# Optimization experiments

Hardware: AMD Instinct MI355X
Metric: run time of the kernel (lower is better)

## Reference

```python
import jax, jax.numpy as jnp
import numpy as np

B, N, S = 8, 4096, 1024          # clouds, points per cloud, fps samples per cloud
C_IN = 64
R_LIST = (0.1, 0.2, 0.4)
K_LIST = (16, 32, 64)
CHANNELS = ([C_IN + 3, 64, 64, 128], [C_IN + 3, 128, 128, 256], [C_IN + 3, 128, 128, 256])


def setup_inputs() -> dict:
    key = jax.random.key(0)
    ks = jax.random.split(key, 2 + 9)
    inp = {}
    inp["x"] = jax.random.normal(ks[0], (B * N, C_IN), jnp.float32)
    inp["pos"] = jax.random.uniform(ks[1], (B * N, 3), jnp.float32)
    inp["batch"] = jnp.repeat(jnp.arange(B, dtype=jnp.int32), N)
    ki = 2
    for s, ch in enumerate(CHANNELS):
        for l in range(len(ch) - 1):
            inp[f"W{s}_{l}"] = jax.random.normal(ks[ki], (ch[l], ch[l + 1]), jnp.float32) / np.float32(np.sqrt(ch[l]))
            inp[f"b{s}_{l}"] = jnp.zeros((ch[l + 1],), jnp.float32)
        ki += 1
    return inp


def _fps_one(pos_b):
    """Farthest point sampling on one cloud [N,3] -> [S] int32 indices (start at 0)."""
    def step(carry, _):
        min_d, last = carry
        d = jnp.sum((pos_b - pos_b[last]) ** 2, axis=-1)          # [N]
        min_d = jnp.minimum(min_d, d)
        return (min_d, jnp.argmax(min_d).astype(jnp.int32)), last
    init = (jnp.full((N,), jnp.inf, pos_b.dtype), jnp.int32(0))
    _, idx = jax.lax.scan(step, init, None, length=S)
    return idx


def _scale(xb, posb, centers, r, K, Ws, bs):
    """Radius ball query (K nearest within r) + PointConv (MLP on [x_j, pos_j-pos_i], max-aggr)."""
    d2 = jnp.sum((centers[:, None, :] - posb[None, :, :]) ** 2, axis=-1)  # [S,N]
    neg = jnp.where(d2 <= r * r, -d2, -jnp.inf)
    vals, nbr = jax.lax.top_k(neg, K)                                      # [S,K]
    valid = vals > -jnp.inf                                                # center itself always valid
    feat = jnp.concatenate([xb[nbr], posb[nbr] - centers[:, None, :]], axis=-1)  # [S,K,C+3]
    h = feat
    for W, b in zip(Ws, bs):
        h = jax.nn.relu(h @ W + b)
    h = jnp.where(valid[..., None], h, -jnp.inf)
    return jnp.max(h, axis=1)                                              # [S,out]


def _forward(x, pos, batch, params):
    xb = x.reshape(B, N, C_IN)
    posb = pos.reshape(B, N, 3)
    idx = jax.vmap(_fps_one)(posb)                                # [B,S]
    centers = jnp.take_along_axis(posb, idx[..., None], axis=1)   # [B,S,3]
    outs = []
    for s in range(3):
        Ws, bs = params[s]
        f = lambda xb_, pb_, c_, Ws=Ws, bs=bs, s=s: _scale(xb_, pb_, c_, R_LIST[s], K_LIST[s], Ws, bs)
        outs.append(jax.vmap(f)(xb, posb, centers))
    new_x = jnp.concatenate(outs, axis=-1).reshape(B * S, -1)     # [B*S, 640]
    new_pos = centers.reshape(B * S, 3)
    new_batch = jnp.repeat(jnp.arange(B, dtype=batch.dtype), S)
    return new_x, new_pos, new_batch


def reference(x, pos, batch, W0_0, b0_0, W0_1, b0_1, W0_2, b0_2,
              W1_0, b1_0, W1_1, b1_1, W1_2, b1_2,
              W2_0, b2_0, W2_1, b2_1, W2_2, b2_2):
    params = (((W0_0, W0_1, W0_2), (b0_0, b0_1, b0_2)),
              ((W1_0, W1_1, W1_2), (b1_0, b1_1, b1_2)),
              ((W2_0, W2_1, W2_2), (b2_0, b2_1, b2_2)))
    return _forward(x, pos, batch, params)
```

## Files before the change

### kernel.cpp

```cpp
#include <hip/hip_runtime.h>

#define NB 8
#define NP 4096
#define NS 1024
#define PROGSTRIDE 32

typedef _Float16 f16x8 __attribute__((ext_vector_type(8)));
typedef _Float16 f16x4 __attribute__((ext_vector_type(4)));
typedef float f32x4 __attribute__((ext_vector_type(4)));

#define DPP_MAX(v, ctrl)                                                     \
    v = fmaxf(v, __int_as_float(__builtin_amdgcn_update_dpp(                 \
                __float_as_int(v), __float_as_int(v), (ctrl), 0xf, 0xf, false)))

struct PrepArgs {
    const float* src[9];
    _Float16* dst[9];
    int kr[9], kp[9], nc[9];
};

template <int K>
__device__ __forceinline__ void select_center(
        const float* __restrict__ pb,
        const float* __restrict__ centers,
        int* __restrict__ nbr, int* __restrict__ nvalid,
        float r2, int scid) {
#pragma clang fp contract(off)
    const int lane = threadIdx.x & 63;
    const unsigned kr2 = __float_as_uint(r2);
    const float cx = centers[scid * 3 + 0];
    const float cy = centers[scid * 3 + 1];
    const float cz = centers[scid * 3 + 2];

    unsigned key[64];
#pragma unroll
    for (int i = 0; i < 64; ++i) {
        const float* pp = pb + (size_t)(lane + i * 64) * 3;
        float dx = pp[0] - cx; float sx = dx * dx;
        float dy = pp[1] - cy; float sy = dy * dy;
        float dz = pp[2] - cz; float sz = dz * dz;
        float d2 = sx + sy; d2 = d2 + sz;
        key[i] = __float_as_uint(d2);
    }

    const unsigned long long below = (1ull << lane) - 1ull;
    int c_cnt = 0;
#pragma unroll
    for (int i = 0; i < 64; ++i)
        c_cnt += __popcll(__ballot(key[i] <= kr2));

    unsigned thr = kr2;
    int nv = c_cnt;
    bool need_ties = false;
    unsigned tkey = 0;
    if (c_cnt > K) {
        nv = K;
        unsigned lo = 0, hi = kr2;
        need_ties = true;
        while (lo < hi) {
            unsigned mid = lo + ((hi - lo) >> 1);
            int cnt = 0;
#pragma unroll
            for (int i = 0; i < 64; ++i)
                cnt += __popcll(__ballot(key[i] <= mid));
            if (cnt == K) { thr = mid; need_ties = false; break; }
            if (cnt > K) hi = mid; else lo = mid + 1;
        }
        tkey = lo;
    }

    if (!need_ties) {
        int base = 0;
#pragma unroll
        for (int i = 0; i < 64; ++i) {
            unsigned long long m = __ballot(key[i] <= thr);
            if (key[i] <= thr)
                nbr[(size_t)scid * K + base + __popcll(m & below)] = lane + i * 64;
            base += __popcll(m);
        }
    } else {
        const unsigned t = tkey;
        int m_cnt = 0;
#pragma unroll
        for (int i = 0; i < 64; ++i)
            m_cnt += __popcll(__ballot(key[i] < t));
        const int rem = K - m_cnt;
        int base = 0, tcnt = 0;
#pragma unroll
        for (int i = 0; i < 64; ++i) {
            unsigned long long lt = __ballot(key[i] < t);
            unsigned long long eq = __ballot(key[i] == t);
            if (key[i] < t) {
                nbr[(size_t)scid * K + base + __popcll(lt & below)] = lane + i * 64;
            } else if (key[i] == t) {
                int tr = tcnt + __popcll(eq & below);
                if (tr < rem) nbr[(size_t)scid * K + (m_cnt + tr)] = lane + i * 64;
            }
            base += __popcll(lt);
            tcnt += __popcll(eq);
        }
    }
    if (lane == 0) nvalid[scid] = nv;
}

__global__ __launch_bounds__(512, 1) void fps_select_fused(
        const float* __restrict__ pos,
        float* __restrict__ centers,
        float* __restrict__ out_pos,
        float* __restrict__ out_batch,
        int* __restrict__ nbr0, int* __restrict__ nbr1, int* __restrict__ nbr2,
        int* __restrict__ nval,
        unsigned* __restrict__ prog,
        PrepArgs pa) {
#pragma clang fp contract(off)
    const int tid = threadIdx.x;
    const int lane = tid & 63;

    if (blockIdx.x < NB) {
        const int b = blockIdx.x;
        const int wid = tid >> 6;
        __shared__ float4 slot[2][8];

        const float* pb = pos + (size_t)b * NP * 3;
        float px[8], py[8], pz[8], md[8];
        {
            const float4* pv = (const float4*)(pb + tid * 24);
            float4 q0 = pv[0], q1 = pv[1], q2 = pv[2];
            float4 q3 = pv[3], q4 = pv[4], q5 = pv[5];
            px[0] = q0.x; py[0] = q0.y; pz[0] = q0.z;
            px[1] = q0.w; py[1] = q1.x; pz[1] = q1.y;
            px[2] = q1.z; py[2] = q1.w; pz[2] = q2.x;
            px[3] = q2.y; py[3] = q2.z; pz[3] = q2.w;
            px[4] = q3.x; py[4] = q3.y; pz[4] = q3.z;
            px[5] = q3.w; py[5] = q4.x; pz[5] = q4.y;
            px[6] = q4.z; py[6] = q4.w; pz[6] = q5.x;
            px[7] = q5.y; py[7] = q5.z; pz[7] = q5.w;
        }
#pragma unroll
        for (int j = 0; j < 8; ++j) md[j] = __builtin_inff();
        for (int t = tid; t < NS; t += 512) out_batch[b * NS + t] = (float)b;

        float cx = pb[0], cy = pb[1], cz = pb[2];
        if (tid == 0) {
            size_t o = (size_t)(b * NS) * 3;
            centers[o + 0] = cx; centers[o + 1] = cy; centers[o + 2] = cz;
            out_pos[o + 0] = cx; out_pos[o + 1] = cy; out_pos[o + 2] = cz;
        }

        int par = 0;
        for (int t = 1; t < NS; ++t) {
            float bv = -1.0f, bx = cx, by = cy, bz = cz;
#pragma unroll
            for (int j = 0; j < 8; ++j) {
                float dx = px[j] - cx; float sx = dx * dx;
                float dy = py[j] - cy; float sy = dy * dy;
                float dz = pz[j] - cz; float sz = dz * dz;
                float d = sx + sy; d = d + sz;
                float m = fminf(md[j], d);
                md[j] = m;
                bool c = m > bv;
                bv = c ? m : bv;
                bx = c ? px[j] : bx;
                by = c ? py[j] : by;
                bz = c ? pz[j] : bz;
            }
            float v = bv;
            DPP_MAX(v, 0x111);
            DPP_MAX(v, 0x112);
            DPP_MAX(v, 0x114);
            DPP_MAX(v, 0x118);
            DPP_MAX(v, 0x142);
            DPP_MAX(v, 0x143);
            const float mx = __int_as_float(
                __builtin_amdgcn_readlane(__float_as_int(v), 63));
            unsigned long long tie = __ballot(bv == mx);
            if (lane == __ffsll(tie) - 1)
                slot[par][wid] = make_float4(mx, bx, by, bz);
            __syncthreads();
            float4 s0 = slot[par][0], s1 = slot[par][1];
            float4 s2 = slot[par][2], s3 = slot[par][3];
            float4 s4 = slot[par][4], s5 = slot[par][5];
            float4 s6 = slot[par][6], s7 = slot[par][7];
            float4 a01 = (s1.x > s0.x) ? s1 : s0;
            float4 a23 = (s3.x > s2.x) ? s3 : s2;
            float4 a45 = (s5.x > s4.x) ? s5 : s4;
            float4 a67 = (s7.x > s6.x) ? s7 : s6;
            float4 b03 = (a23.x > a01.x) ? a23 : a01;
            float4 b47 = (a67.x > a45.x) ? a67 : a45;
            float4 wn = (b47.x > b03.x) ? b47 : b03;
            cx = wn.y; cy = wn.z; cz = wn.w;
            if (tid == 0) {
                size_t o = (size_t)(b * NS + t) * 3;
                centers[o + 0] = cx; centers[o + 1] = cy; centers[o + 2] = cz;
                out_pos[o + 0] = cx; out_pos[o + 1] = cy; out_pos[o + 2] = cz;
                if ((t & 15) == 15)
                    __hip_atomic_store(&prog[b * PROGSTRIDE], (unsigned)(t + 1),
                                       __ATOMIC_RELEASE, __HIP_MEMORY_SCOPE_AGENT);
            }
            par ^= 1;
        }
    } else {
        const int wblk = blockIdx.x - NB;
        {
            const int wtid = wblk * 512 + tid;
            const int NW = 248 * 512;
#pragma unroll 1
            for (int m = 0; m < 9; ++m) {
                const int kp = pa.kp[m], kr = pa.kr[m], nc = pa.nc[m];
                const float* src = pa.src[m];
                _Float16* dst = pa.dst[m];
                const int tot = kp * nc;
                for (int i = wtid; i < tot; i += NW) {
                    int n = i / kp, k = i - n * kp;
                    dst[i] = (k < kr) ? (_Float16)src[(size_t)k * nc + n]
                                      : (_Float16)0.f;
                }
            }
        }
        const int wid = tid >> 6;
        const int wave_id = wblk * 8 + wid;
        const int NWAVE = 248 * 8;
        const int NTASK = 3 * NB * NS;
        for (int T = wave_id; T < NTASK; T += NWAVE) {
            const int s = T / 24;
            const int r = T - s * 24;
            const int b = r & 7;
            const int seg = r >> 3;
            const int scid = b * NS + s;
            while (__hip_atomic_load(&prog[b * PROGSTRIDE], __ATOMIC_ACQUIRE,
                                     __HIP_MEMORY_SCOPE_AGENT) <= (unsigned)s)
                __builtin_amdgcn_s_sleep(32);
            const float* pb = pos + (size_t)b * NP * 3;
            if (seg == 0)
                select_center<16>(pb, centers, nbr0, nval,
                                  (float)(0.1 * 0.1), scid);
            else if (seg == 1)
                select_center<32>(pb, centers, nbr1, nval + 8192,
                                  (float)(0.2 * 0.2), scid);
            else
                select_center<64>(pb, centers, nbr2, nval + 16384,
                                  (float)(0.4 * 0.4), scid);
        }
    }
}

template <int KN, int CPB, int C1, int C2, int C3, int OFF, int NCTR>
__device__ void mlp_body(
        char* smem,
        const float* __restrict__ x, const float* __restrict__ pos,
        const float* __restrict__ centers,
        const int* __restrict__ nbr, const int* __restrict__ nvalid,
        const _Float16* __restrict__ wt1, const _Float16* __restrict__ wt2,
        const _Float16* __restrict__ wt3,
        const float* __restrict__ b1, const float* __restrict__ b2,
        const float* __restrict__ b3,
        float* __restrict__ out, int blk) {
    constexpr int M = KN * CPB;
    constexpr int K1P = 96;
    constexpr int S1 = K1P + 8;
    constexpr int S2 = C1 + 8;
    constexpr int S3 = C2 + 8;
    constexpr int MT = M / 16;
    constexpr int NCH1 = C1 / 4, NCH2 = C2 / 4, NCH3 = C3 / 4;
    constexpr int NT1 = NCH1 / 16, NT2 = NCH2 / 16, NT3 = NCH3 / 16;
    constexpr int KT1 = K1P / 32, KT2 = C1 / 32, KT3 = C2 / 32;
    constexpr int NBATCH = NCTR / CPB;

    _Float16* feat = (_Float16*)smem;
    _Float16* h1 = feat + M * S1;
    _Float16* h2 = h1 + M * S2;
    int* outmax = (int*)(h2 + M * S3);

    const int tid = threadIdx.x;
    const int lane = tid & 63;
    const int w = tid >> 6;
    const int lm = lane & 15;
    const int lq = lane >> 4;

    f16x8 wf1[NT1][KT1], wf2[NT2][KT2], wf3[NT3][KT3];
    float bb1[NT1], bb2[NT2], bb3[NT3];
#pragma unroll
    for (int nt = 0; nt < NT1; ++nt) {
        int n = w * NCH1 + nt * 16 + lm;
        bb1[nt] = b1[n];
#pragma unroll
        for (int kt = 0; kt < KT1; ++kt)
            wf1[nt][kt] = *(const f16x8*)(wt1 + (size_t)n * K1P + kt * 32 + lq * 8);
    }
#pragma unroll
    for (int nt = 0; nt < NT2; ++nt) {
        int n = w * NCH2 + nt * 16 + lm;
        bb2[nt] = b2[n];
#pragma unroll
        for (int kt = 0; kt < KT2; ++kt)
            wf2[nt][kt] = *(const f16x8*)(wt2 + (size_t)n * C1 + kt * 32 + lq * 8);
    }
#pragma unroll
    for (int nt = 0; nt < NT3; ++nt) {
        int n = w * NCH3 + nt * 16 + lm;
        bb3[nt] = b3[n];
#pragma unroll
        for (int kt = 0; kt < KT3; ++kt)
            wf3[nt][kt] = *(const f16x8*)(wt3 + (size_t)n * C2 + kt * 32 + lq * 8);
    }

    for (int bt = 0; bt < NBATCH; ++bt) {
        const int cid0 = blk * NCTR + bt * CPB;
        __syncthreads();

        for (int i = tid; i < CPB * C3; i += 256) outmax[i] = 0;

        for (int it = tid; it < M * 16; it += 256) {
            const int r = it >> 4, sub = it & 15;
            const int c = r / KN, lr = r - c * KN;
            const int cid = cid0 + c;
            if (lr < nvalid[cid]) {
                int pt = nbr[(size_t)cid * KN + lr];
                float4 v = *(const float4*)(x + ((size_t)((cid >> 10) * NP) + pt) * 64 + sub * 4);
                f16x4 hv = {(_Float16)v.x, (_Float16)v.y, (_Float16)v.z, (_Float16)v.w};
                *(f16x4*)(feat + r * S1 + sub * 4) = hv;
            }
        }
        for (int it = tid; it < M * 4; it += 256) {
            const int r = it >> 2, q = it & 3;
            const int c = r / KN, lr = r - c * KN;
            const int cid = cid0 + c;
            f16x8 z = {(_Float16)0.f, (_Float16)0.f, (_Float16)0.f, (_Float16)0.f,
                       (_Float16)0.f, (_Float16)0.f, (_Float16)0.f, (_Float16)0.f};
            if (q == 0 && lr < nvalid[cid]) {
                int pt = nbr[(size_t)cid * KN + lr];
                const float* pr = pos + ((size_t)((cid >> 10) * NP) + pt) * 3;
                z[0] = (_Float16)(pr[0] - centers[cid * 3 + 0]);
                z[1] = (_Float16)(pr[1] - centers[cid * 3 + 1]);
                z[2] = (_Float16)(pr[2] - centers[cid * 3 + 2]);
            }
            *(f16x8*)(feat + r * S1 + 64 + q * 8) = z;
        }
        __syncthreads();

#pragma unroll
        for (int mt = 0; mt < MT; ++mt) {
            f16x8 a[KT1];
#pragma unroll
            for (int kt = 0; kt < KT1; ++kt)
                a[kt] = *(const f16x8*)(feat + (mt * 16 + lm) * S1 + kt * 32 + lq * 8);
#pragma unroll
            for (int nt = 0; nt < NT1; ++nt) {
                f32x4 acc = {bb1[nt], bb1[nt], bb1[nt], bb1[nt]};
#pragma unroll
                for (int kt = 0; kt < KT1; ++kt)
                    acc = __builtin_amdgcn_mfma_f32_16x16x32_f16(a[kt], wf1[nt][kt], acc, 0, 0, 0);
                const int gc = w * NCH1 + nt * 16 + lm;
#pragma unroll
                for (int rg = 0; rg < 4; ++rg)
                    h1[(mt * 16 + lq * 4 + rg) * S2 + gc] = (_Float16)fmaxf(acc[rg], 0.f);
            }
        }
        __syncthreads();

#pragma unroll
        for (int mt = 0; mt < MT; ++mt) {
            f16x8 a[KT2];
#pragma unroll
            for (int kt = 0; kt < KT2; ++kt)
                a[kt] = *(const f16x8*)(h1 + (mt * 16 + lm) * S2 + kt * 32 + lq * 8);
#pragma unroll
            for (int nt = 0; nt < NT2; ++nt) {
                f32x4 acc = {bb2[nt], bb2[nt], bb2[nt], bb2[nt]};
#pragma unroll
                for (int kt = 0; kt < KT2; ++kt)
                    acc = __builtin_amdgcn_mfma_f32_16x16x32_f16(a[kt], wf2[nt][kt], acc, 0, 0, 0);
                const int gc = w * NCH2 + nt * 16 + lm;
#pragma unroll
                for (int rg = 0; rg < 4; ++rg)
                    h2[(mt * 16 + lq * 4 + rg) * S3 + gc] = (_Float16)fmaxf(acc[rg], 0.f);
            }
        }
        __syncthreads();

#pragma unroll
        for (int mt = 0; mt < MT; ++mt) {
            constexpr int TPC = KN / 16;
            const int c = mt / TPC;
            const int nv = nvalid[cid0 + c];
            const int lr0 = (mt % TPC) * 16;
            f16x8 a[KT3];
#pragma unroll
            for (int kt = 0; kt < KT3; ++kt)
                a[kt] = *(const f16x8*)(h2 + (mt * 16 + lm) * S3 + kt * 32 + lq * 8);
#pragma unroll
            for (int nt = 0; nt < NT3; ++nt) {
                f32x4 acc = {bb3[nt], bb3[nt], bb3[nt], bb3[nt]};
#pragma unroll
                for (int kt = 0; kt < KT3; ++kt)
                    acc = __builtin_amdgcn_mfma_f32_16x16x32_f16(a[kt], wf3[nt][kt], acc, 0, 0, 0);
                float mx = -1.f;
#pragma unroll
                for (int rg = 0; rg < 4; ++rg) {
                    int lr = lr0 + lq * 4 + rg;
                    float v = fmaxf(acc[rg], 0.f);
                    if (lr < nv) mx = fmaxf(mx, v);
                }
                mx = fmaxf(mx, __shfl_xor(mx, 16));
                mx = fmaxf(mx, __shfl_xor(mx, 32));
                if (lane < 16)
                    atomicMax(&outmax[c * C3 + w * NCH3 + nt * 16 + lm],
                              __float_as_int(mx));
            }
        }
        __syncthreads();
        for (int i = tid; i < CPB * C3; i += 256) {
            const int c = i / C3, j = i - c * C3;
            out[(size_t)(cid0 + c) * 640 + OFF + j] = __int_as_float(outmax[i]);
        }
    }
}

struct MlpW {
    const _Float16* w[9];
    const float* bias[9];
};

__global__ __launch_bounds__(256, 2) void mlp_all(
        const float* __restrict__ x, const float* __restrict__ pos,
        const float* __restrict__ centers,
        const int* __restrict__ nbr0, const int* __restrict__ nbr1,
        const int* __restrict__ nbr2, const int* __restrict__ nval,
        MlpW ww, float* __restrict__ out) {
    extern __shared__ char smem[];
    const int blk = blockIdx.x;
    const int sblk = blk & 1023;
    const int eblk = (sblk & 7) * 128 + (sblk >> 3);
    if (blk < 1024)
        mlp_body<16, 4, 64, 64, 128, 0, 8>(smem, x, pos, centers, nbr0, nval,
            ww.w[0], ww.w[1], ww.w[2], ww.bias[0], ww.bias[1], ww.bias[2], out, eblk);
    else if (blk < 2048)
        mlp_body<32, 2, 128, 128, 256, 128, 8>(smem, x, pos, centers, nbr1, nval + 8192,
            ww.w[3], ww.w[4], ww.w[5], ww.bias[3], ww.bias[4], ww.bias[5], out, eblk);
    else
        mlp_body<64, 1, 128, 128, 256, 384, 8>(smem, x, pos, centers, nbr2, nval + 16384,
            ww.w[6], ww.w[7], ww.w[8], ww.bias[6], ww.bias[7], ww.bias[8], out, eblk);
}

extern "C" void kernel_launch(void* const* d_in, const int* in_sizes, int n_in,
                              void* d_out, int out_size, void* d_ws, size_t ws_size,
                              hipStream_t stream) {
    const float* x = (const float*)d_in[0];
    const float* pos = (const float*)d_in[1];
    const float* W0_0 = (const float*)d_in[3];
    const float* b0_0 = (const float*)d_in[4];
    const float* W0_1 = (const float*)d_in[5];
    const float* b0_1 = (const float*)d_in[6];
    const float* W0_2 = (const float*)d_in[7];
    const float* b0_2 = (const float*)d_in[8];
    const float* W1_0 = (const float*)d_in[9];
    const float* b1_0 = (const float*)d_in[10];
    const float* W1_1 = (const float*)d_in[11];
    const float* b1_1 = (const float*)d_in[12];
    const float* W1_2 = (const float*)d_in[13];
    const float* b1_2 = (const float*)d_in[14];
    const float* W2_0 = (const float*)d_in[15];
    const float* b2_0 = (const float*)d_in[16];
    const float* W2_1 = (const float*)d_in[17];
    const float* b2_1 = (const float*)d_in[18];
    const float* W2_2 = (const float*)d_in[19];
    const float* b2_2 = (const float*)d_in[20];

    float* out = (float*)d_out;
    char* ws = (char*)d_ws;
    float* centers = (float*)(ws + 0);
    int* nbr0 = (int*)(ws + 98304);
    int* nbr1 = (int*)(ws + 622592);
    int* nbr2 = (int*)(ws + 1671168);
    int* nval = (int*)(ws + 3768320);
    _Float16* w0t1 = (_Float16*)(ws + 3866624);
    _Float16* w0t2 = (_Float16*)(ws + 3878912);
    _Float16* w0t3 = (_Float16*)(ws + 3887104);
    _Float16* w1t1 = (_Float16*)(ws + 3903488);
    _Float16* w1t2 = (_Float16*)(ws + 3928064);
    _Float16* w1t3 = (_Float16*)(ws + 3960832);
    _Float16* w2t1 = (_Float16*)(ws + 4026368);
    _Float16* w2t2 = (_Float16*)(ws + 4050944);
    _Float16* w2t3 = (_Float16*)(ws + 4083712);
    unsigned* prog = (unsigned*)(ws + 4149248);

    float* out_pos = out + (size_t)8192 * 640;
    float* out_batch = out_pos + (size_t)8192 * 3;

    hipMemsetAsync(prog, 0, NB * PROGSTRIDE * sizeof(unsigned), stream);

    PrepArgs pa;
    pa.src[0] = W0_0; pa.dst[0] = w0t1; pa.kr[0] = 67;  pa.kp[0] = 96;  pa.nc[0] = 64;
    pa.src[1] = W0_1; pa.dst[1] = w0t2; pa.kr[1] = 64;  pa.kp[1] = 64;  pa.nc[1] = 64;
    pa.src[2] = W0_2; pa.dst[2] = w0t3; pa.kr[2] = 64;  pa.kp[2] = 64;  pa.nc[2] = 128;
    pa.src[3] = W1_0; pa.dst[3] = w1t1; pa.kr[3] = 67;  pa.kp[3] = 96;  pa.nc[3] = 128;
    pa.src[4] = W1_1; pa.dst[4] = w1t2; pa.kr[4] = 128; pa.kp[4] = 128; pa.nc[4] = 128;
    pa.src[5] = W1_2; pa.dst[5] = w1t3; pa.kr[5] = 128; pa.kp[5] = 128; pa.nc[5] = 256;
    pa.src[6] = W2_0; pa.dst[6] = w2t1; pa.kr[6] = 67;  pa.kp[6] = 96;  pa.nc[6] = 128;
    pa.src[7] = W2_1; pa.dst[7] = w2t2; pa.kr[7] = 128; pa.kp[7] = 128; pa.nc[7] = 128;
    pa.src[8] = W2_2; pa.dst[8] = w2t3; pa.kr[8] = 128; pa.kp[8] = 128; pa.nc[8] = 256;

    fps_select_fused<<<dim3(256), dim3(512), 0, stream>>>(
        pos, centers, out_pos, out_batch, nbr0, nbr1, nbr2, nval, prog, pa);

    MlpW ww;
    ww.w[0] = w0t1; ww.w[1] = w0t2; ww.w[2] = w0t3;
    ww.w[3] = w1t1; ww.w[4] = w1t2; ww.w[5] = w1t3;
    ww.w[6] = w2t1; ww.w[7] = w2t2; ww.w[8] = w2t3;
    ww.bias[0] = b0_0; ww.bias[1] = b0_1; ww.bias[2] = b0_2;
    ww.bias[3] = b1_0; ww.bias[4] = b1_1; ww.bias[5] = b1_2;
    ww.bias[6] = b2_0; ww.bias[7] = b2_1; ww.bias[8] = b2_2;

    mlp_all<<<dim3(3072), dim3(256), 50176, stream>>>(
        x, pos, centers, nbr0, nbr1, nbr2, nval, ww, out);
}
```

Before: 1.098 ms.

## Pre-convert point features to fp16 and stage neighbor indices in LDS

The idle worker blocks of the FPS kernel now convert x to fp16 into workspace while FPS runs, so the MLP gather reads half the bytes with 16-byte loads. The MLP kernel also stages neighbor indices and valid counts into shared memory once per batch instead of rereading them from global memory for every element. The fp16 path runs only if the workspace is large enough, and the extra conversion work competes with the neighbor-select tasks in the fused kernel. Shared memory per block grows slightly.

```diff
diff --git a/kernel.cpp b/kernel.cpp
--- a/kernel.cpp
+++ b/kernel.cpp
@@ -4,6 +4,8 @@
 #define NP 4096
 #define NS 1024
 #define PROGSTRIDE 32
+#define XH_OFF 4150272
+#define XH_BYTES (NB * NP * 64 * 2)
 
 typedef _Float16 f16x8 __attribute__((ext_vector_type(8)));
 typedef _Float16 f16x4 __attribute__((ext_vector_type(4)));
@@ -111,7 +113,9 @@
         int* __restrict__ nbr0, int* __restrict__ nbr1, int* __restrict__ nbr2,
         int* __restrict__ nval,
         unsigned* __restrict__ prog,
-        PrepArgs pa) {
+        PrepArgs pa,
+        const float* __restrict__ x,
+        _Float16* __restrict__ xh) {
 #pragma clang fp contract(off)
     const int tid = threadIdx.x;
     const int lane = tid & 63;
@@ -216,6 +220,17 @@
                                       : (_Float16)0.f;
                 }
             }
+            if (xh) {
+                const float4* xs = (const float4*)x;
+                f16x4* xd = (f16x4*)xh;
+                const int tot = NB * NP * 64 / 4;
+                for (int i = wtid; i < tot; i += NW) {
+                    float4 v = xs[i];
+                    f16x4 h = {(_Float16)v.x, (_Float16)v.y,
+                               (_Float16)v.z, (_Float16)v.w};
+                    xd[i] = h;
+                }
+            }
         }
         const int wid = tid >> 6;
         const int wave_id = wblk * 8 + wid;
@@ -247,7 +262,8 @@
 template <int KN, int CPB, int C1, int C2, int C3, int OFF, int NCTR>
 __device__ void mlp_body(
         char* smem,
-        const float* __restrict__ x, const float* __restrict__ pos,
+        const float* __restrict__ x, const _Float16* __restrict__ xh,
+        const float* __restrict__ pos,
         const float* __restrict__ centers,
         const int* __restrict__ nbr, const int* __restrict__ nvalid,
         const _Float16* __restrict__ wt1, const _Float16* __restrict__ wt2,
@@ -270,6 +286,8 @@
     _Float16* h1 = feat + M * S1;
     _Float16* h2 = h1 + M * S2;
     int* outmax = (int*)(h2 + M * S3);
+    int* nbuf = outmax + CPB * C3;
+    int* nvbuf = nbuf + M;
 
     const int tid = threadIdx.x;
     const int lane = tid & 63;
@@ -309,16 +327,35 @@
         __syncthreads();
 
         for (int i = tid; i < CPB * C3; i += 256) outmax[i] = 0;
-
-        for (int it = tid; it < M * 16; it += 256) {
-            const int r = it >> 4, sub = it & 15;
-            const int c = r / KN, lr = r - c * KN;
-            const int cid = cid0 + c;
-            if (lr < nvalid[cid]) {
-                int pt = nbr[(size_t)cid * KN + lr];
-                float4 v = *(const float4*)(x + ((size_t)((cid >> 10) * NP) + pt) * 64 + sub * 4);
-                f16x4 hv = {(_Float16)v.x, (_Float16)v.y, (_Float16)v.z, (_Float16)v.w};
-                *(f16x4*)(feat + r * S1 + sub * 4) = hv;
+        for (int i = tid; i < M; i += 256) {
+            const int c = i / KN;
+            nbuf[i] = nbr[(size_t)(cid0 + c) * KN + (i - c * KN)];
+        }
+        if (tid < CPB) nvbuf[tid] = nvalid[cid0 + tid];
+        __syncthreads();
+
+        if (xh) {
+            for (int it = tid; it < M * 8; it += 256) {
+                const int r = it >> 3, sub = it & 7;
+                const int c = r / KN, lr = r - c * KN;
+                if (lr < nvbuf[c]) {
+                    int pt = nbuf[r];
+                    f16x8 hv = *(const f16x8*)(
+                        xh + ((size_t)((((cid0 + c) >> 10)) * NP) + pt) * 64 + sub * 8);
+                    *(f16x8*)(feat + r * S1 + sub * 8) = hv;
+                }
+            }
+        } else {
+            for (int it = tid; it < M * 16; it += 256) {
+                const int r = it >> 4, sub = it & 15;
+                const int c = r / KN, lr = r - c * KN;
+                if (lr < nvbuf[c]) {
+                    int pt = nbuf[r];
+                    float4 v = *(const float4*)(
+                        x + ((size_t)((((cid0 + c) >> 10)) * NP) + pt) * 64 + sub * 4);
+                    f16x4 hv = {(_Float16)v.x, (_Float16)v.y, (_Float16)v.z, (_Float16)v.w};
+                    *(f16x4*)(feat + r * S1 + sub * 4) = hv;
+                }
             }
         }
         for (int it = tid; it < M * 4; it += 256) {
@@ -327,8 +364,8 @@
             const int cid = cid0 + c;
             f16x8 z = {(_Float16)0.f, (_Float16)0.f, (_Float16)0.f, (_Float16)0.f,
                        (_Float16)0.f, (_Float16)0.f, (_Float16)0.f, (_Float16)0.f};
-            if (q == 0 && lr < nvalid[cid]) {
-                int pt = nbr[(size_t)cid * KN + lr];
+            if (q == 0 && lr < nvbuf[c]) {
+                int pt = nbuf[r];
                 const float* pr = pos + ((size_t)((cid >> 10) * NP) + pt) * 3;
                 z[0] = (_Float16)(pr[0] - centers[cid * 3 + 0]);
                 z[1] = (_Float16)(pr[1] - centers[cid * 3 + 1]);
@@ -382,7 +419,7 @@
         for (int mt = 0; mt < MT; ++mt) {
             constexpr int TPC = KN / 16;
             const int c = mt / TPC;
-            const int nv = nvalid[cid0 + c];
+            const int nv = nvbuf[c];
             const int lr0 = (mt % TPC) * 16;
             f16x8 a[KT3];
 #pragma unroll
@@ -422,7 +459,8 @@
 };
 
 __global__ __launch_bounds__(256, 2) void mlp_all(
-        const float* __restrict__ x, const float* __restrict__ pos,
+        const float* __restrict__ x, const _Float16* __restrict__ xh,
+        const float* __restrict__ pos,
         const float* __restrict__ centers,
         const int* __restrict__ nbr0, const int* __restrict__ nbr1,
         const int* __restrict__ nbr2, const int* __restrict__ nval,
@@ -432,13 +470,13 @@
     const int sblk = blk & 1023;
     const int eblk = (sblk & 7) * 128 + (sblk >> 3);
     if (blk < 1024)
-        mlp_body<16, 4, 64, 64, 128, 0, 8>(smem, x, pos, centers, nbr0, nval,
+        mlp_body<16, 4, 64, 64, 128, 0, 8>(smem, x, xh, pos, centers, nbr0, nval,
             ww.w[0], ww.w[1], ww.w[2], ww.bias[0], ww.bias[1], ww.bias[2], out, eblk);
     else if (blk < 2048)
-        mlp_body<32, 2, 128, 128, 256, 128, 8>(smem, x, pos, centers, nbr1, nval + 8192,
+        mlp_body<32, 2, 128, 128, 256, 128, 8>(smem, x, xh, pos, centers, nbr1, nval + 8192,
             ww.w[3], ww.w[4], ww.w[5], ww.bias[3], ww.bias[4], ww.bias[5], out, eblk);
     else
-        mlp_body<64, 1, 128, 128, 256, 384, 8>(smem, x, pos, centers, nbr2, nval + 16384,
+        mlp_body<64, 1, 128, 128, 256, 384, 8>(smem, x, xh, pos, centers, nbr2, nval + 16384,
             ww.w[6], ww.w[7], ww.w[8], ww.bias[6], ww.bias[7], ww.bias[8], out, eblk);
 }
 
@@ -483,6 +521,8 @@
     _Float16* w2t2 = (_Float16*)(ws + 4050944);
     _Float16* w2t3 = (_Float16*)(ws + 4083712);
     unsigned* prog = (unsigned*)(ws + 4149248);
+    _Float16* xh = (ws_size >= (size_t)XH_OFF + XH_BYTES)
+                       ? (_Float16*)(ws + XH_OFF) : (_Float16*)0;
 
     float* out_pos = out + (size_t)8192 * 640;
     float* out_batch = out_pos + (size_t)8192 * 3;
@@ -501,7 +541,8 @@
     pa.src[8] = W2_2; pa.dst[8] = w2t3; pa.kr[8] = 128; pa.kp[8] = 128; pa.nc[8] = 256;
 
     fps_select_fused<<<dim3(256), dim3(512), 0, stream>>>(
-        pos, centers, out_pos, out_batch, nbr0, nbr1, nbr2, nval, prog, pa);
+        pos, centers, out_pos, out_batch, nbr0, nbr1, nbr2, nval, prog, pa,
+        x, xh);
 
     MlpW ww;
     ww.w[0] = w0t1; ww.w[1] = w0t2; ww.w[2] = w0t3;
@@ -511,6 +552,6 @@
     ww.bias[3] = b1_0; ww.bias[4] = b1_1; ww.bias[5] = b1_2;
     ww.bias[6] = b2_0; ww.bias[7] = b2_1; ww.bias[8] = b2_2;
 
-    mlp_all<<<dim3(3072), dim3(256), 50176, stream>>>(
-        x, pos, centers, nbr0, nbr1, nbr2, nval, ww, out);
+    mlp_all<<<dim3(3072), dim3(256), 50448, stream>>>(
+        x, xh, pos, centers, nbr0, nbr1, nbr2, nval, ww, out);
 }
```

After: 1.070 ms, median of 2. 1.03x faster.
